# Optimization experiments

Hardware: AMD Instinct MI355X
Metric: run time of the kernel (lower is better)

Reference implementation:

```python
import jax, jax.numpy as jnp
import numpy as np

B, TS, TW = 32, 16, 16
SENT_H, WORD_H, CDIM, WDIM = 256, 512, 32, 300
VOCAB, ABJAD = 50000, 48
DIN = 2 * SENT_H   # sentence-encoder output dim
DQ = 2 * WORD_H    # word(char)-encoder output dim
DEC_H = 2 * WORD_H
DEC_IN = DIN + DQ + 8


def _lstm_dir(x, Wx, Wh, b, reverse=False):
    # x: [N, T, Din]; Wx: [4H, Din]; Wh: [4H, H]; gates ordered i,f,g,o
    pre = jnp.einsum('btd,gd->btg', x, Wx) + b
    N, H = x.shape[0], Wh.shape[1]
    h0 = jnp.zeros((N, H), x.dtype)
    def step(carry, g_in):
        h, c = carry
        g = g_in + h @ Wh.T
        i, f, gg, o = jnp.split(g, 4, axis=-1)
        c = jax.nn.sigmoid(f) * c + jax.nn.sigmoid(i) * jnp.tanh(gg)
        h = jax.nn.sigmoid(o) * jnp.tanh(c)
        return (h, c), h
    _, hs = jax.lax.scan(step, (h0, h0), jnp.swapaxes(pre, 0, 1), reverse=reverse)
    return jnp.swapaxes(hs, 0, 1)


def _bidir(x, Wx, Wh, b):
    return jnp.concatenate([_lstm_dir(x, Wx[0], Wh[0], b[0], False),
                            _lstm_dir(x, Wx[1], Wh[1], b[1], True)], axis=-1)


def setup_inputs():
    key = jax.random.key(0)
    ks = iter(jax.random.split(key, 40))
    def w(shape):
        return jax.random.normal(next(ks), shape, jnp.float32) * 0.02
    inp = {}
    inp['sents'] = jax.random.randint(next(ks), (B, TS), 0, VOCAB)
    inp['words'] = jax.random.randint(next(ks), (B, TS, TW), 0, ABJAD)
    inp['labels'] = jax.random.randint(next(ks), (B, TS, TW, 8), 0, 2)
    inp['word_embs'] = w((VOCAB, WDIM))
    inp['char_table'] = w((ABJAD, CDIM)).at[0].set(0.0)  # padding_idx=0
    inp['sent_Wx0'] = w((2, 4 * SENT_H, WDIM))
    inp['sent_Wh0'] = w((2, 4 * SENT_H, SENT_H))
    inp['sent_b0'] = jnp.zeros((2, 4 * SENT_H), jnp.float32)
    inp['sent_Wx1'] = w((2, 4 * SENT_H, 2 * SENT_H))
    inp['sent_Wh1'] = w((2, 4 * SENT_H, SENT_H))
    inp['sent_b1'] = jnp.zeros((2, 4 * SENT_H), jnp.float32)
    inp['word_Wx0'] = w((2, 4 * WORD_H, CDIM + DIN))
    inp['word_Wh0'] = w((2, 4 * WORD_H, WORD_H))
    inp['word_b0'] = jnp.zeros((2, 4 * WORD_H), jnp.float32)
    inp['word_Wx1'] = w((2, 4 * WORD_H, 2 * WORD_H))
    inp['word_Wh1'] = w((2, 4 * WORD_H, WORD_H))
    inp['word_b1'] = jnp.zeros((2, 4 * WORD_H), jnp.float32)
    inp['attn_Wq'] = w((DQ, DIN))
    inp['dec_Wx'] = w((4 * DEC_H, DEC_IN))
    inp['dec_Wh'] = w((4 * DEC_H, DEC_H))
    inp['dec_b'] = jnp.zeros((4 * DEC_H,), jnp.float32)
    inp['cls_W'] = w((DEC_H, 15))
    inp['cls_b'] = jnp.zeros((15,), jnp.float32)
    return inp


def reference(sents, words, labels, word_embs, char_table, sent_Wx0, sent_Wh0, sent_b0, sent_Wx1, sent_Wh1, sent_b1, word_Wx0, word_Wh0, word_b0, word_Wx1, word_Wh1, word_b1, attn_Wq, dec_Wx, dec_Wh, dec_b, cls_W, cls_b):
    Bb = sents.shape[0]
    word_mask = (words != 0).astype(jnp.float32)               # [B, TS, TW]
    wembs = word_embs[sents]                                   # [B, TS, 300]
    h = _bidir(wembs, sent_Wx0, sent_Wh0, sent_b0)
    sent_enc = _bidir(h, sent_Wx1, sent_Wh1, sent_b1)          # [B, TS, DIN]
    sentword = sent_enc[:, :, None, :] * word_mask[..., None]  # [B, TS, TW, DIN]
    cembs = char_table[words]                                  # [B, TS, TW, CDIM]
    char_in = jnp.concatenate([cembs, sentword], axis=-1).reshape(Bb * TS, TW, CDIM + DIN)
    h = _bidir(char_in, word_Wx0, word_Wh0, word_b0)
    char_enc = _bidir(h, word_Wx1, word_Wh1, word_b1)          # [B*TS, TW, DQ]
    char_enc_r = char_enc.reshape(Bb, TS, TW, DQ)
    # dot attention: char queries projected into sentence-encoding space, keys = sent_enc
    q = jnp.einsum('bicq,qd->bicd', char_enc_r, attn_Wq)
    scores = jnp.einsum('bicd,bjd->bicj', q, sent_enc)         # [B, TS, TW, TS]
    key_valid = (words != 0).any(-1)                           # [B, TS]
    omit_self = ~jnp.eye(TS, dtype=bool)                       # prejudice mask
    valid = key_valid[:, None, None, :] & omit_self[None, :, None, :]
    attn_map = jax.nn.softmax(jnp.where(valid, scores, -1e9), axis=-1)
    attn_enc = jnp.einsum('bicj,bjd->bicd', attn_map, sent_enc)  # [B, TS, TW, DIN]
    final = jnp.concatenate([attn_enc, char_enc_r, labels.astype(jnp.float32)], axis=-1)
    final = final.reshape(Bb, TS * TW, DEC_IN)
    dec_out = _lstm_dir(final, dec_Wx, dec_Wh, dec_b)          # [B, TS*TW, DEC_H]
    diac = dec_out @ cls_W + cls_b
    return diac.reshape(Bb, TS, TW, 15), attn_map
```

## Files before the change

kernel.cpp:

```cpp
#include <hip/hip_runtime.h>
#include <math.h>


typedef __attribute__((ext_vector_type(8))) __bf16 bf16x8;
typedef __attribute__((ext_vector_type(4))) float f32x4;
typedef __attribute__((ext_vector_type(4))) unsigned u32x4;

__device__ __forceinline__ float sigf(float x) { return 1.0f / (1.0f + expf(-x)); }

__device__ __forceinline__ unsigned short bf16rn(float x) {
  unsigned u = __float_as_uint(x);
  return (unsigned short)((u + 0x7fffu + ((u >> 16) & 1u)) >> 16);
}
__device__ __forceinline__ void splitf(float x, unsigned short& h, unsigned short& l) {
  h = bf16rn(x);
  float fh = __uint_as_float((unsigned)h << 16);
  l = bf16rn(x - fh);
}

__device__ __forceinline__ void ldg16_cc(u32x4& d, const void* p) {
  asm volatile("global_load_dwordx4 %0, %1, off sc0 sc1" : "=v"(d) : "v"(p));
}

#define FMA16(a, b, acc)                                                           \
  acc[0][0] += a.x * b.x; acc[0][1] += a.x * b.y; acc[0][2] += a.x * b.z; acc[0][3] += a.x * b.w; \
  acc[1][0] += a.y * b.x; acc[1][1] += a.y * b.y; acc[1][2] += a.y * b.z; acc[1][3] += a.y * b.w; \
  acc[2][0] += a.z * b.x; acc[2][1] += a.z * b.y; acc[2][2] += a.z * b.z; acc[2][3] += a.z * b.w; \
  acc[3][0] += a.w * b.x; acc[3][1] += a.w * b.y; acc[3][2] += a.w * b.z; acc[3][3] += a.w * b.w;

__global__ __launch_bounds__(256) void transpose_k(const float* __restrict__ in,
                                                   float* __restrict__ out,
                                                   int R, int C, int H) {
  __shared__ float tile[32][33];
  int r0 = blockIdx.x * 32, c0 = blockIdx.y * 32;
  int tx = threadIdx.x & 31, ty = threadIdx.x >> 5;
  for (int yy = ty; yy < 32; yy += 8) {
    int r = r0 + yy, c = c0 + tx;
    float v = 0.f;
    if (r < R && c < C) {
      int gs = H ? ((r & 3) * H + (r >> 2)) : r;
      v = in[(long)gs * C + c];
    }
    tile[yy][tx] = v;
  }
  __syncthreads();
  for (int yy = ty; yy < 32; yy += 8) {
    int c = c0 + yy, r = r0 + tx;
    if (r < R && c < C) out[(long)c * R + r] = tile[tx][yy];
  }
}

__global__ void embed_k(const int* __restrict__ sents, const float* __restrict__ word_embs,
                        float* __restrict__ wembs) {
  int idx = blockIdx.x * 256 + threadIdx.x;
  if (idx >= 512 * 300) return;
  int r = idx / 300, k = idx - r * 300;
  wembs[idx] = word_embs[(long)sents[r] * 300 + k];
}

__global__ void charin_k(const int* __restrict__ words, const float* __restrict__ char_table,
                         const float* __restrict__ sent_enc,
                         unsigned short* __restrict__ ciH, unsigned short* __restrict__ ciL) {
  int idx = blockIdx.x * 256 + threadIdx.x;
  if (idx >= 512 * 16 * 544) return;
  int k = idx % 544;
  int rc = idx / 544;
  int c = rc & 15, n = rc >> 4;
  int w = words[n * 16 + c];
  float v;
  if (k < 32) v = char_table[w * 32 + k];
  else v = (w != 0) ? sent_enc[n * 512 + (k - 32)] : 0.f;
  unsigned short h, l;
  splitf(v, h, l);
  ciH[idx] = h; ciL[idx] = l;
}

__global__ void labels_k(const int* __restrict__ labels,
                         unsigned short* __restrict__ fH, unsigned short* __restrict__ fL) {
  int idx = blockIdx.x * 256 + threadIdx.x;
  if (idx >= 8192 * 8) return;
  int r = idx >> 3, l = idx & 7;
  long o = (long)r * 1544 + 1536 + l;
  fH[o] = bf16rn((float)labels[idx]);
  fL[o] = 0;
}

__global__ void decwh_prep_k(const float* __restrict__ dec_Wh,
                             unsigned short* __restrict__ WhFH,
                             unsigned short* __restrict__ WhFL) {
  long o = (long)blockIdx.x * 256 + threadIdx.x;
  if (o >= 4194304) return;
  int j = (int)(o & 7);
  int lane = (int)((o >> 3) & 63);
  int kt = (int)((o >> 9) & 31);
  int nt = (int)(o >> 14);
  int col = nt * 16 + (lane & 15);
  int gsrc = (col & 3) * 1024 + (col >> 2);
  int k = kt * 32 + ((lane >> 4) & 3) * 8 + j;
  float v = dec_Wh[(long)gsrc * 1024 + k];
  unsigned short h, l;
  splitf(v, h, l);
  WhFH[o] = h; WhFL[o] = l;
}

template <int HASBIAS>
__global__ __launch_bounds__(256) void gemm_k(const float* __restrict__ A, int lda,
                                              const float* __restrict__ Bw,
                                              const float* __restrict__ bias,
                                              float* __restrict__ C, int ldc,
                                              int M, int N, int K) {
  __shared__ float As[32][64];
  __shared__ float Bs[32][64];
  int tid = threadIdx.x;
  int m0 = blockIdx.x * 64, n0 = blockIdx.y * 64;
  int tn = tid & 15, tm = tid >> 4;
  int lrow = tid >> 2, lk = (tid & 3) * 8;
  float acc[4][4] = {};
  int am = m0 + lrow;
  const float* aptr = A + (long)am * lda;
  bool mok = am < M;
  int bn = n0 + lrow;
  const float* bptr = Bw + (long)bn * K;
  bool nok = bn < N;

  for (int k0 = 0; k0 < K; k0 += 32) {
    int kb = k0 + lk;
    if (kb + 8 <= K) {
      if (mok) {
        float4 v0 = *(const float4*)(aptr + kb);
        float4 v1 = *(const float4*)(aptr + kb + 4);
        As[lk + 0][lrow] = v0.x; As[lk + 1][lrow] = v0.y; As[lk + 2][lrow] = v0.z; As[lk + 3][lrow] = v0.w;
        As[lk + 4][lrow] = v1.x; As[lk + 5][lrow] = v1.y; As[lk + 6][lrow] = v1.z; As[lk + 7][lrow] = v1.w;
      } else {
#pragma unroll
        for (int i = 0; i < 8; i++) As[lk + i][lrow] = 0.f;
      }
      if (nok) {
        float4 v0 = *(const float4*)(bptr + kb);
        float4 v1 = *(const float4*)(bptr + kb + 4);
        Bs[lk + 0][lrow] = v0.x; Bs[lk + 1][lrow] = v0.y; Bs[lk + 2][lrow] = v0.z; Bs[lk + 3][lrow] = v0.w;
        Bs[lk + 4][lrow] = v1.x; Bs[lk + 5][lrow] = v1.y; Bs[lk + 6][lrow] = v1.z; Bs[lk + 7][lrow] = v1.w;
      } else {
#pragma unroll
        for (int i = 0; i < 8; i++) Bs[lk + i][lrow] = 0.f;
      }
    } else {
#pragma unroll
      for (int i = 0; i < 8; i++) {
        int k = kb + i;
        As[lk + i][lrow] = (mok && k < K) ? aptr[k] : 0.f;
        Bs[lk + i][lrow] = (nok && k < K) ? bptr[k] : 0.f;
      }
    }
    __syncthreads();
#pragma unroll
    for (int kk = 0; kk < 32; kk++) {
      float4 a = *(const float4*)&As[kk][tm * 4];
      float4 b = *(const float4*)&Bs[kk][tn * 4];
      FMA16(a, b, acc)
    }
    __syncthreads();
  }
#pragma unroll
  for (int i = 0; i < 4; i++) {
    int m = m0 + tm * 4 + i;
    if (m >= M) continue;
#pragma unroll
    for (int j = 0; j < 4; j++) {
      int n = n0 + tn * 4 + j;
      if (n >= N) continue;
      float v = acc[i][j];
      if (HASBIAS) v += bias[n];
      C[(long)m * ldc + n] = v;
    }
  }
}

template <int AMODE, int BH, int HASBIAS>
__global__ __launch_bounds__(256) void mgemm_k(const unsigned short* __restrict__ AH,
                                               const unsigned short* __restrict__ AL,
                                               int lda, int at0,
                                               const float* __restrict__ B,
                                               const float* __restrict__ bias,
                                               float* __restrict__ C, int ldc, int K) {
  __shared__ __align__(16) unsigned short Ah[64 * 40], Al[64 * 40], Bh[64 * 40], Bl[64 * 40];
  int tid = threadIdx.x;
  int m0 = blockIdx.x * 64, n0 = blockIdx.y * 64;
  int srow = tid >> 2, skoff = (tid & 3) * 8;
  int am = m0 + srow;
  long arow = (AMODE == 1) ? ((long)(am & 31) * 256 + at0 + (am >> 5)) : (long)am;
  const unsigned short* aptrH = AH + arow * (long)lda;
  const unsigned short* aptrL = AL + arow * (long)lda;
  int bn = n0 + srow;
  long gsrc;
  if (BH > 0) gsrc = (long)(bn & 3) * BH + (bn >> 2);
  else gsrc = bn;
  const float* bptr = B + gsrc * (long)K;

  int lane = tid & 63, wv = tid >> 6;
  int wm = (wv >> 1) * 32, wn = (wv & 1) * 32;
  int fr = lane & 15, fk = (lane >> 4) * 8;
  int rbase = (lane >> 4) * 4;

  f32x4 acc[2][2] = {};
  for (int k0 = 0; k0 < K; k0 += 32) {
    int kb = k0 + skoff;
    uint4 vh, vl;
    unsigned short hb[8] __attribute__((aligned(16))), lb[8] __attribute__((aligned(16)));
    if (kb + 8 <= K) {
      vh = *(const uint4*)(aptrH + kb);
      vl = *(const uint4*)(aptrL + kb);
      float4 b0 = *(const float4*)(bptr + kb);
      float4 b1 = *(const float4*)(bptr + kb + 4);
      float bv[8] = {b0.x, b0.y, b0.z, b0.w, b1.x, b1.y, b1.z, b1.w};
#pragma unroll
      for (int e = 0; e < 8; e++) splitf(bv[e], hb[e], lb[e]);
    } else {
      unsigned short ea[8] __attribute__((aligned(16))), el[8] __attribute__((aligned(16)));
#pragma unroll
      for (int e = 0; e < 8; e++) {
        int k = kb + e;
        ea[e] = (k < K) ? aptrH[k] : 0;
        el[e] = (k < K) ? aptrL[k] : 0;
        float bvv = (k < K) ? bptr[k] : 0.f;
        splitf(bvv, hb[e], lb[e]);
      }
      vh = *(const uint4*)ea;
      vl = *(const uint4*)el;
    }
    __syncthreads();
    *(uint4*)&Ah[srow * 40 + skoff] = vh;
    *(uint4*)&Al[srow * 40 + skoff] = vl;
    *(uint4*)&Bh[srow * 40 + skoff] = *(const uint4*)hb;
    *(uint4*)&Bl[srow * 40 + skoff] = *(const uint4*)lb;
    __syncthreads();
    bf16x8 fah[2], fal[2], fbh[2], fbl[2];
#pragma unroll
    for (int i = 0; i < 2; i++) {
      fah[i] = *(const bf16x8*)&Ah[(wm + i * 16 + fr) * 40 + fk];
      fal[i] = *(const bf16x8*)&Al[(wm + i * 16 + fr) * 40 + fk];
      fbh[i] = *(const bf16x8*)&Bh[(wn + i * 16 + fr) * 40 + fk];
      fbl[i] = *(const bf16x8*)&Bl[(wn + i * 16 + fr) * 40 + fk];
    }
#pragma unroll
    for (int i = 0; i < 2; i++)
#pragma unroll
      for (int j = 0; j < 2; j++) {
        acc[i][j] = __builtin_amdgcn_mfma_f32_16x16x32_bf16(fah[i], fbh[j], acc[i][j], 0, 0, 0);
        acc[i][j] = __builtin_amdgcn_mfma_f32_16x16x32_bf16(fah[i], fbl[j], acc[i][j], 0, 0, 0);
        acc[i][j] = __builtin_amdgcn_mfma_f32_16x16x32_bf16(fal[i], fbh[j], acc[i][j], 0, 0, 0);
      }
  }
#pragma unroll
  for (int i = 0; i < 2; i++)
#pragma unroll
    for (int j = 0; j < 2; j++)
#pragma unroll
      for (int r = 0; r < 4; r++) {
        int m = m0 + wm + i * 16 + rbase + r;
        int n = n0 + wn + j * 16 + fr;
        float v = acc[i][j][r];
        if (HASBIAS) {
          long gs = (BH > 0) ? ((long)(n & 3) * BH + (n >> 2)) : (long)n;
          v += bias[gs];
        }
        C[(long)m * ldc + n] = v;
      }
}

template <int K1>
__global__ __launch_bounds__(256) void mstep_k(
    const unsigned short* __restrict__ xFH, const unsigned short* __restrict__ xFL,
    const unsigned short* __restrict__ xBH, const unsigned short* __restrict__ xBL,
    int xstride,
    const float* __restrict__ Wx, const float* __restrict__ Wh,
    const float* __restrict__ bias,
    const unsigned short* __restrict__ hInH, const unsigned short* __restrict__ hInL,
    unsigned short* __restrict__ hOutH, unsigned short* __restrict__ hOutL,
    float* __restrict__ c_st,
    unsigned short* __restrict__ outH, unsigned short* __restrict__ outL,
    int out_stride, int tF, int tB) {
  __shared__ __align__(16) char smem[20480];
  unsigned short* Ah = (unsigned short*)smem;
  unsigned short* Al = Ah + 2560;
  unsigned short* Bh = Ah + 5120;
  unsigned short* Bl = Ah + 7680;
  float* gbuf = (float*)smem;

  int tid = threadIdx.x;
  int m0 = blockIdx.x * 64, n0 = blockIdx.y * 64;
  int dir = n0 >> 11;
  int nn0 = n0 & 2047;
  int srow = tid >> 2, skoff = (tid & 3) * 8;

  int am = m0 + srow;
  const unsigned short* axH = dir ? xBH : xFH;
  const unsigned short* axL = dir ? xBL : xFL;
  const unsigned short* arow_xH = axH + (long)am * xstride;
  const unsigned short* arow_xL = axL + (long)am * xstride;
  const unsigned short* arow_hH = hInH + (long)dir * 262144 + (long)am * 512;
  const unsigned short* arow_hL = hInL + (long)dir * 262144 + (long)am * 512;

  int bn = nn0 + srow;
  long gsrc = (long)dir * 2048 + (bn & 3) * 512 + (bn >> 2);
  const float* brow_x = Wx + gsrc * (long)K1;
  const float* brow_h = Wh + gsrc * 512L;

  int lane = tid & 63, wv = tid >> 6;
  int wm = (wv >> 1) * 32, wn = (wv & 1) * 32;
  int fr = lane & 15, fk = (lane >> 4) * 8;
  int rbase = (lane >> 4) * 4;

  f32x4 acc[2][2] = {};
  const int K = K1 + 512;
  for (int k0 = 0; k0 < K; k0 += 32) {
    int kb = k0 + skoff;
    uint4 vh, vl;
    const float* bp;
    if (kb < K1) {
      vh = *(const uint4*)(arow_xH + kb);
      vl = *(const uint4*)(arow_xL + kb);
      bp = brow_x + kb;
    } else {
      vh = *(const uint4*)(arow_hH + (kb - K1));
      vl = *(const uint4*)(arow_hL + (kb - K1));
      bp = brow_h + (kb - K1);
    }
    float4 b0 = *(const float4*)bp;
    float4 b1 = *(const float4*)(bp + 4);
    float bv[8] = {b0.x, b0.y, b0.z, b0.w, b1.x, b1.y, b1.z, b1.w};
    unsigned short hb[8] __attribute__((aligned(16))), lb[8] __attribute__((aligned(16)));
#pragma unroll
    for (int e = 0; e < 8; e++) splitf(bv[e], hb[e], lb[e]);
    __syncthreads();
    *(uint4*)&Ah[srow * 40 + skoff] = vh;
    *(uint4*)&Al[srow * 40 + skoff] = vl;
    *(uint4*)&Bh[srow * 40 + skoff] = *(const uint4*)hb;
    *(uint4*)&Bl[srow * 40 + skoff] = *(const uint4*)lb;
    __syncthreads();
    bf16x8 fah[2], fal[2], fbh[2], fbl[2];
#pragma unroll
    for (int i = 0; i < 2; i++) {
      fah[i] = *(const bf16x8*)&Ah[(wm + i * 16 + fr) * 40 + fk];
      fal[i] = *(const bf16x8*)&Al[(wm + i * 16 + fr) * 40 + fk];
      fbh[i] = *(const bf16x8*)&Bh[(wn + i * 16 + fr) * 40 + fk];
      fbl[i] = *(const bf16x8*)&Bl[(wn + i * 16 + fr) * 40 + fk];
    }
#pragma unroll
    for (int i = 0; i < 2; i++)
#pragma unroll
      for (int j = 0; j < 2; j++) {
        acc[i][j] = __builtin_amdgcn_mfma_f32_16x16x32_bf16(fah[i], fbh[j], acc[i][j], 0, 0, 0);
        acc[i][j] = __builtin_amdgcn_mfma_f32_16x16x32_bf16(fah[i], fbl[j], acc[i][j], 0, 0, 0);
        acc[i][j] = __builtin_amdgcn_mfma_f32_16x16x32_bf16(fal[i], fbh[j], acc[i][j], 0, 0, 0);
      }
  }
  __syncthreads();
#pragma unroll
  for (int i = 0; i < 2; i++)
#pragma unroll
    for (int j = 0; j < 2; j++)
#pragma unroll
      for (int r = 0; r < 4; r++)
        gbuf[(wm + i * 16 + rbase + r) * 68 + (wn + j * 16 + fr)] = acc[i][j][r];
  __syncthreads();

  int ug0 = nn0 >> 2;
  int t = dir ? tB : tF;
  for (int it = tid; it < 1024; it += 256) {
    int r = it >> 4, ul = it & 15;
    int seq = m0 + r, ug = ug0 + ul;
    float gi = gbuf[r * 68 + ul * 4 + 0] + bias[dir * 2048 + ug];
    float gf = gbuf[r * 68 + ul * 4 + 1] + bias[dir * 2048 + 512 + ug];
    float gg = gbuf[r * 68 + ul * 4 + 2] + bias[dir * 2048 + 1024 + ug];
    float go = gbuf[r * 68 + ul * 4 + 3] + bias[dir * 2048 + 1536 + ug];
    long ci = (long)dir * 262144 + (long)seq * 512 + ug;
    float c = sigf(gf) * c_st[ci] + sigf(gi) * tanhf(gg);
    float h = sigf(go) * tanhf(c);
    c_st[ci] = c;
    unsigned short hh, hl;
    splitf(h, hh, hl);
    hOutH[ci] = hh;
    hOutL[ci] = hl;
    long oo = ((long)seq * 16 + t) * out_stride + dir * 512 + ug;
    outH[oo] = hh;
    outL[oo] = hl;
  }
}

__global__ __launch_bounds__(256) void sent_rec_k(const float* __restrict__ pre,
                                                  const float* __restrict__ WhT,
                                                  float* __restrict__ out) {
  int blk = blockIdx.x;
  int n = blk & 31, dir = blk >> 5;
  int tid = threadIdx.x;
  __shared__ float hls[256];
  __shared__ float gls[1024];
  float c = 0.f;
  hls[tid] = 0.f;
  __syncthreads();
  const float* whbase = WhT + (long)dir * 256 * 1024;
  int g4 = tid * 4;
  for (int s = 0; s < 16; s++) {
    int t = dir ? (15 - s) : s;
    const float* prow = pre + (long)(n * 16 + t) * 2048 + dir * 1024;
    float ax = 0.f, ay = 0.f, az = 0.f, aw = 0.f;
#pragma unroll 4
    for (int k = 0; k < 256; k++) {
      float hk = hls[k];
      float4 w = *(const float4*)(whbase + (long)k * 1024 + g4);
      ax += hk * w.x; ay += hk * w.y; az += hk * w.z; aw += hk * w.w;
    }
    float4 p = *(const float4*)(prow + g4);
    gls[g4 + 0] = ax + p.x; gls[g4 + 1] = ay + p.y;
    gls[g4 + 2] = az + p.z; gls[g4 + 3] = aw + p.w;
    __syncthreads();
    float gi = gls[tid], gf = gls[256 + tid], gg = gls[512 + tid], go = gls[768 + tid];
    c = sigf(gf) * c + sigf(gi) * tanhf(gg);
    float h = sigf(go) * tanhf(c);
    __syncthreads();
    hls[tid] = h;
    out[(long)n * 8192 + (long)t * 512 + dir * 256 + tid] = h;
    __syncthreads();
  }
}

__global__ __launch_bounds__(256, 1) void dec_persist_k(
    const unsigned short* __restrict__ WhFH, const unsigned short* __restrict__ WhFL,
    const float* __restrict__ pre,
    unsigned short* __restrict__ hH, unsigned short* __restrict__ hL,
    float* __restrict__ c_st, float* __restrict__ dec_out,
    int* __restrict__ cnt, int tbase) {
  extern __shared__ char smem[];
  unsigned short* wHs = (unsigned short*)smem;
  unsigned short* wLs = (unsigned short*)(smem + 65536);
  float* gbuf = (float*)(smem + 131072);

  int tid = threadIdx.x, bid = blockIdx.x;
  int lane = tid & 63, kh = tid >> 6;
  int fr = lane & 15, fq = (lane >> 4) & 3;
  int grp = bid >> 3;

  {
    const unsigned short* gH = WhFH + (long)bid * 32768;
    const unsigned short* gL = WhFL + (long)bid * 32768;
    for (int o = tid * 8; o < 32768; o += 2048) {
      *(uint4*)&wHs[o] = *(const uint4*)&gH[o];
      *(uint4*)&wLs[o] = *(const uint4*)&gL[o];
    }
  }

  int bb = tid >> 2, up = tid & 3;
  int u0 = bid * 8 + up * 2;
  long co = (long)bb * 1024 + u0;
  float c0 = 0.f, c1 = 0.f;
  if (tid < 128) {
    float2 cc = *(const float2*)&c_st[co];
    c0 = cc.x;
    c1 = cc.y;
  }
  __syncthreads();

  for (int tl = 0; tl < 32; tl++) {
    int t = tbase + tl;
    const unsigned short* hInH = hH + (long)(t & 1) * 32768;
    const unsigned short* hInL = hL + (long)(t & 1) * 32768;
    unsigned short* hOutH = hH + (long)((t + 1) & 1) * 32768;
    unsigned short* hOutL = hL + (long)((t + 1) & 1) * 32768;

    float4 p0 = {0.f, 0.f, 0.f, 0.f}, p1 = {0.f, 0.f, 0.f, 0.f};
    if (tid < 128) {
      const float* pr = pre + ((long)tl * 32 + bb) * 4096 + bid * 32 + up * 8;
      p0 = *(const float4*)pr;
      p1 = *(const float4*)(pr + 4);
    }

    u32x4 hHr[2][8], hLr[2][8];
#pragma unroll
    for (int bh = 0; bh < 2; bh++)
#pragma unroll
      for (int i = 0; i < 8; i++) {
        long a = (long)(bh * 16 + fr) * 1024 + (kh * 8 + i) * 32 + fq * 8;
        ldg16_cc(hHr[bh][i], hInH + a);
        ldg16_cc(hLr[bh][i], hInL + a);
      }
    asm volatile("s_waitcnt vmcnt(0)");
    __builtin_amdgcn_sched_barrier(0);

    f32x4 acc[2][2] = {};
#pragma unroll
    for (int i = 0; i < 8; i++) {
      int kt = kh * 8 + i;
#pragma unroll
      for (int ct = 0; ct < 2; ct++) {
        bf16x8 wh = *(const bf16x8*)&wHs[(ct * 32 + kt) * 512 + lane * 8];
        bf16x8 wl = *(const bf16x8*)&wLs[(ct * 32 + kt) * 512 + lane * 8];
#pragma unroll
        for (int bh = 0; bh < 2; bh++) {
          bf16x8 ah = __builtin_bit_cast(bf16x8, hHr[bh][i]);
          bf16x8 al = __builtin_bit_cast(bf16x8, hLr[bh][i]);
          acc[ct][bh] = __builtin_amdgcn_mfma_f32_16x16x32_bf16(ah, wh, acc[ct][bh], 0, 0, 0);
          acc[ct][bh] = __builtin_amdgcn_mfma_f32_16x16x32_bf16(ah, wl, acc[ct][bh], 0, 0, 0);
          acc[ct][bh] = __builtin_amdgcn_mfma_f32_16x16x32_bf16(al, wh, acc[ct][bh], 0, 0, 0);
        }
      }
    }
#pragma unroll
    for (int ct = 0; ct < 2; ct++)
#pragma unroll
      for (int bh = 0; bh < 2; bh++)
#pragma unroll
        for (int r = 0; r < 4; r++)
          gbuf[(kh * 32 + bh * 16 + fq * 4 + r) * 33 + ct * 16 + fr] = acc[ct][bh][r];
    __syncthreads();

    if (tid < 128) {
      float g[8];
#pragma unroll
      for (int e = 0; e < 8; e++) {
        float s = gbuf[bb * 33 + up * 8 + e];
#pragma unroll
        for (int q = 1; q < 4; q++) s += gbuf[(q * 32 + bb) * 33 + up * 8 + e];
        g[e] = s;
      }
      c0 = sigf(g[1] + p0.y) * c0 + sigf(g[0] + p0.x) * tanhf(g[2] + p0.z);
      float h0 = sigf(g[3] + p0.w) * tanhf(c0);
      c1 = sigf(g[5] + p1.y) * c1 + sigf(g[4] + p1.x) * tanhf(g[6] + p1.z);
      float h1 = sigf(g[7] + p1.w) * tanhf(c1);
      unsigned short h0h, h0l, h1h, h1l;
      splitf(h0, h0h, h0l);
      splitf(h1, h1h, h1l);
      unsigned ph = (unsigned)h0h | ((unsigned)h1h << 16);
      unsigned pl = (unsigned)h0l | ((unsigned)h1l << 16);
      __hip_atomic_store((unsigned*)(hOutH + co), ph, __ATOMIC_RELAXED,
                         __HIP_MEMORY_SCOPE_AGENT);
      __hip_atomic_store((unsigned*)(hOutL + co), pl, __ATOMIC_RELAXED,
                         __HIP_MEMORY_SCOPE_AGENT);
      float2 hv;
      hv.x = h0;
      hv.y = h1;
      *(float2*)&dec_out[((long)bb * 256 + t) * 1024 + u0] = hv;
    }
    __syncthreads();

    if (tl < 31) {
      if (tid == 0) {
        int old = __hip_atomic_fetch_add(&cnt[grp * 32], 1, __ATOMIC_RELAXED,
                                         __HIP_MEMORY_SCOPE_AGENT);
        if (old == 8 * tl + 7)
          __hip_atomic_fetch_add(&cnt[512], 1, __ATOMIC_RELAXED,
                                 __HIP_MEMORY_SCOPE_AGENT);
        while (__hip_atomic_load(&cnt[512], __ATOMIC_RELAXED,
                                 __HIP_MEMORY_SCOPE_AGENT) < 16 * (tl + 1))
          __builtin_amdgcn_s_sleep(1);
      }
      __syncthreads();
    }
  }
  if (tid < 128) {
    float2 cv;
    cv.x = c0;
    cv.y = c1;
    *(float2*)&c_st[co] = cv;
  }
}

__global__ __launch_bounds__(256) void attn_k(const float* __restrict__ sent_enc,
                                              const float* __restrict__ qbuf,
                                              const int* __restrict__ words,
                                              float* __restrict__ attn_out,
                                              unsigned short* __restrict__ fH,
                                              unsigned short* __restrict__ fL) {
  int b = blockIdx.x >> 4;
  int i = blockIdx.x & 15;
  int tid = threadIdx.x;
  __shared__ float se[16][512];
  __shared__ float qq[16][512];
  __shared__ float sc[16][16];
  __shared__ int kv[16];
  if (tid < 16) kv[tid] = 0;
  __syncthreads();
  {
    int j = tid >> 4, c = tid & 15;
    if (words[(b * 16 + j) * 16 + c] != 0) atomicOr(&kv[j], 1);
  }
  for (int idx = tid; idx < 16 * 128; idx += 256) {
    int j = idx >> 7, d4 = idx & 127;
    *(float4*)&se[j][d4 * 4] = *(const float4*)(sent_enc + (long)(b * 16 + j) * 512 + d4 * 4);
  }
  for (int idx = tid; idx < 16 * 128; idx += 256) {
    int c = idx >> 7, d4 = idx & 127;
    *(float4*)&qq[c][d4 * 4] = *(const float4*)(qbuf + (long)(b * 256 + i * 16 + c) * 512 + d4 * 4);
  }
  __syncthreads();
  int c = tid >> 4, j = tid & 15;
  {
    float s = 0.f;
#pragma unroll 4
    for (int k = 0; k < 512; k++) s += qq[c][k] * se[j][k];
    bool valid = (kv[j] != 0) && (j != i);
    sc[c][j] = valid ? s : -1e9f;
  }
  __syncthreads();
  float m = -INFINITY;
#pragma unroll
  for (int t = 0; t < 16; t++) m = fmaxf(m, sc[c][t]);
  float den = 0.f;
#pragma unroll
  for (int t = 0; t < 16; t++) den += expf(sc[c][t] - m);
  float a = expf(sc[c][j] - m) / den;
  __syncthreads();
  sc[c][j] = a;
  attn_out[((long)((b * 16 + i) * 16 + c)) * 16 + j] = a;
  __syncthreads();
  {
    int part = tid & 15;
    int cc = tid >> 4;
    for (int d = part * 32; d < part * 32 + 32; d++) {
      float v = 0.f;
#pragma unroll
      for (int jj = 0; jj < 16; jj++) v += sc[cc][jj] * se[jj][d];
      long o = (long)(b * 256 + i * 16 + cc) * 1544 + d;
      unsigned short hh, hl;
      splitf(v, hh, hl);
      fH[o] = hh;
      fL[o] = hl;
    }
  }
}

extern "C" void kernel_launch(void* const* d_in, const int* in_sizes, int n_in,
                              void* d_out, int out_size, void* d_ws, size_t ws_size,
                              hipStream_t stream) {
  const int* sents = (const int*)d_in[0];
  const int* words = (const int*)d_in[1];
  const int* labels = (const int*)d_in[2];
  const float* word_embs = (const float*)d_in[3];
  const float* char_table = (const float*)d_in[4];
  const float* sent_Wx0 = (const float*)d_in[5];
  const float* sent_Wh0 = (const float*)d_in[6];
  const float* sent_b0 = (const float*)d_in[7];
  const float* sent_Wx1 = (const float*)d_in[8];
  const float* sent_Wh1 = (const float*)d_in[9];
  const float* sent_b1 = (const float*)d_in[10];
  const float* word_Wx0 = (const float*)d_in[11];
  const float* word_Wh0 = (const float*)d_in[12];
  const float* word_b0 = (const float*)d_in[13];
  const float* word_Wx1 = (const float*)d_in[14];
  const float* word_Wh1 = (const float*)d_in[15];
  const float* word_b1 = (const float*)d_in[16];
  const float* attn_Wq = (const float*)d_in[17];
  const float* dec_Wx = (const float*)d_in[18];
  const float* dec_Wh = (const float*)d_in[19];
  const float* dec_b = (const float*)d_in[20];
  const float* cls_W = (const float*)d_in[21];
  const float* cls_b = (const float*)d_in[22];

  char* base = (char*)d_ws;
  float* wembs   = (float*)(base + 0);
  float* preS    = (float*)(base + 614400);
  float* hs0     = (float*)(base + 4808704);
  float* WhT0    = (float*)(base + 5857280);
  float* WhT1    = (float*)(base + 7954432);
  float* sentenc = (float*)(base + 10051584);
  unsigned short* hcharH = (unsigned short*)(base + 11100160);
  unsigned short* hcharL = (unsigned short*)(base + 13197312);
  float* cchar   = (float*)(base + 15294464);
  unsigned short* WhFH = (unsigned short*)(base + 0);
  unsigned short* WhFL = (unsigned short*)(base + 8388608);
  unsigned short* finalbH = (unsigned short*)(base + 17391616);
  unsigned short* finalbL = (unsigned short*)(base + 42688512);
  float* qbuf = (float*)(base + 67985408);
  float* pre  = qbuf;
  float* WqT = (float*)(base + 84762624);
  unsigned short* charinH = (unsigned short*)(base + 86859776);
  unsigned short* charinL = (unsigned short*)(base + 95772672);
  unsigned short* hc0H = (unsigned short*)(base + 104685568);
  unsigned short* hc0L = (unsigned short*)(base + 121462784);
  float* dec_out = (float*)(base + 86859776);
  unsigned short* hdecH = (unsigned short*)(base + 120414208);
  unsigned short* hdecL = (unsigned short*)(base + 120545280);
  float* c_dec = (float*)(base + 120676352);
  float* clsWT = (float*)(base + 120807424);
  int* cnt = (int*)(base + 120868864);

  float* dout = (float*)d_out;
  float* diac = dout;
  float* attnmap = dout + 122880;

  static bool s_dec_attr = false;
  if (!s_dec_attr) {
    hipFuncSetAttribute(reinterpret_cast<const void*>(dec_persist_k),
                        hipFuncAttributeMaxDynamicSharedMemorySize, 147968);
    s_dec_attr = true;
  }

  transpose_k<<<dim3(32, 8), 256, 0, stream>>>(sent_Wh0, WhT0, 1024, 256, 0);
  transpose_k<<<dim3(32, 8), 256, 0, stream>>>(sent_Wh0 + 262144, WhT0 + 262144, 1024, 256, 0);
  transpose_k<<<dim3(32, 8), 256, 0, stream>>>(sent_Wh1, WhT1, 1024, 256, 0);
  transpose_k<<<dim3(32, 8), 256, 0, stream>>>(sent_Wh1 + 262144, WhT1 + 262144, 1024, 256, 0);
  transpose_k<<<dim3(32, 16), 256, 0, stream>>>(attn_Wq, WqT, 1024, 512, 0);

  embed_k<<<600, 256, 0, stream>>>(sents, word_embs, wembs);
  gemm_k<1><<<dim3(8, 32), 256, 0, stream>>>(wembs, 300, sent_Wx0, sent_b0,
                                             preS, 2048, 512, 2048, 300);
  sent_rec_k<<<64, 256, 0, stream>>>(preS, WhT0, hs0);
  gemm_k<1><<<dim3(8, 32), 256, 0, stream>>>(hs0, 512, sent_Wx1, sent_b1,
                                             preS, 2048, 512, 2048, 512);
  sent_rec_k<<<64, 256, 0, stream>>>(preS, WhT1, sentenc);

  charin_k<<<17408, 256, 0, stream>>>(words, char_table, sentenc, charinH, charinL);

  hipMemsetAsync(base + 11100160, 0, 6291456, stream);
  for (int s = 0; s < 16; s++) {
    int p = s & 1;
    mstep_k<544><<<dim3(8, 64), 256, 0, stream>>>(
        charinH + s * 544, charinL + s * 544,
        charinH + (15 - s) * 544, charinL + (15 - s) * 544, 16 * 544,
        word_Wx0, word_Wh0, word_b0,
        hcharH + p * 524288, hcharL + p * 524288,
        hcharH + (p ^ 1) * 524288, hcharL + (p ^ 1) * 524288, cchar,
        hc0H, hc0L, 1024, s, 15 - s);
  }
  hipMemsetAsync(base + 11100160, 0, 6291456, stream);
  for (int s = 0; s < 16; s++) {
    int p = s & 1;
    mstep_k<1024><<<dim3(8, 64), 256, 0, stream>>>(
        hc0H + s * 1024, hc0L + s * 1024,
        hc0H + (15 - s) * 1024, hc0L + (15 - s) * 1024, 16 * 1024,
        word_Wx1, word_Wh1, word_b1,
        hcharH + p * 524288, hcharL + p * 524288,
        hcharH + (p ^ 1) * 524288, hcharL + (p ^ 1) * 524288, cchar,
        finalbH + 512, finalbL + 512, 1544, s, 15 - s);
  }

  mgemm_k<0, 0, 0><<<dim3(128, 8), 256, 0, stream>>>(finalbH + 512, finalbL + 512, 1544, 0,
                                                     WqT, nullptr, qbuf, 512, 1024);
  attn_k<<<512, 256, 0, stream>>>(sentenc, qbuf, words, attnmap, finalbH, finalbL);
  labels_k<<<256, 256, 0, stream>>>(labels, finalbH, finalbL);

  decwh_prep_k<<<16384, 256, 0, stream>>>(dec_Wh, WhFH, WhFL);
  hipMemsetAsync(base + 120414208, 0, 393216, stream);
  for (int ch = 0; ch < 8; ch++) {
    mgemm_k<1, 1024, 1><<<dim3(16, 64), 256, 0, stream>>>(finalbH, finalbL, 1544, ch * 32,
                                                          dec_Wx, dec_b, pre, 4096, 1544);
    hipMemsetAsync(cnt, 0, 4096, stream);
    dec_persist_k<<<128, 256, 147968, stream>>>(WhFH, WhFL, pre, hdecH, hdecL,
                                                c_dec, dec_out, cnt, ch * 32);
  }

  transpose_k<<<dim3(32, 1), 256, 0, stream>>>(cls_W, clsWT, 1024, 15, 0);
  gemm_k<1><<<dim3(128, 1), 256, 0, stream>>>(dec_out, 1024, clsWT, cls_b,
                                              diac, 15, 8192, 15, 1024);
}
```

Before: 4.701 ms.

## Shrink decoder persistent grid to 32 larger blocks reading Wh from global

The decoder recurrence kernel moves from 128 blocks of 256 threads, each holding its Wh slice in LDS, to 32 blocks of 512 threads that each handle four times as many hidden units. Weights are now read from global memory (L2) every timestep instead of being staged in LDS. The grid barrier drops from a two-level counter to a single counter over 32 blocks. The aim is cheaper cross-block synchronisation per step, at the cost of re-reading the full Wh from cache every step and running on fewer CUs.

Result: slower. 7.208 ms (+53.3%).

```diff
diff --git a/kernel.cpp b/kernel.cpp
--- a/kernel.cpp
+++ b/kernel.cpp
@@ -425,41 +425,26 @@
   }
 }
 
-__global__ __launch_bounds__(256, 1) void dec_persist_k(
+__global__ __launch_bounds__(512, 2) void dec_persist_k(
     const unsigned short* __restrict__ WhFH, const unsigned short* __restrict__ WhFL,
     const float* __restrict__ pre,
     unsigned short* __restrict__ hH, unsigned short* __restrict__ hL,
     float* __restrict__ c_st, float* __restrict__ dec_out,
     int* __restrict__ cnt, int tbase) {
   extern __shared__ char smem[];
-  unsigned short* wHs = (unsigned short*)smem;
-  unsigned short* wLs = (unsigned short*)(smem + 65536);
-  float* gbuf = (float*)(smem + 131072);
+  float* gbuf = (float*)smem;
 
   int tid = threadIdx.x, bid = blockIdx.x;
   int lane = tid & 63, kh = tid >> 6;
   int fr = lane & 15, fq = (lane >> 4) & 3;
-  int grp = bid >> 3;
-
-  {
-    const unsigned short* gH = WhFH + (long)bid * 32768;
-    const unsigned short* gL = WhFL + (long)bid * 32768;
-    for (int o = tid * 8; o < 32768; o += 2048) {
-      *(uint4*)&wHs[o] = *(const uint4*)&gH[o];
-      *(uint4*)&wLs[o] = *(const uint4*)&gL[o];
-    }
-  }
-
-  int bb = tid >> 2, up = tid & 3;
-  int u0 = bid * 8 + up * 2;
+
+  int bb = tid >> 4, up = tid & 15;
+  int u0 = bid * 32 + up * 2;
   long co = (long)bb * 1024 + u0;
-  float c0 = 0.f, c1 = 0.f;
-  if (tid < 128) {
-    float2 cc = *(const float2*)&c_st[co];
-    c0 = cc.x;
-    c1 = cc.y;
-  }
-  __syncthreads();
+  float2 cc = *(const float2*)&c_st[co];
+  float c0 = cc.x, c1 = cc.y;
+
+  const long wfb = ((long)(bid * 8) * 32 + kh * 4) * 512 + lane * 8;
 
   for (int tl = 0; tl < 32; tl++) {
     int t = tbase + tl;
@@ -468,33 +453,32 @@
     unsigned short* hOutH = hH + (long)((t + 1) & 1) * 32768;
     unsigned short* hOutL = hL + (long)((t + 1) & 1) * 32768;
 
-    float4 p0 = {0.f, 0.f, 0.f, 0.f}, p1 = {0.f, 0.f, 0.f, 0.f};
-    if (tid < 128) {
-      const float* pr = pre + ((long)tl * 32 + bb) * 4096 + bid * 32 + up * 8;
-      p0 = *(const float4*)pr;
-      p1 = *(const float4*)(pr + 4);
-    }
-
-    u32x4 hHr[2][8], hLr[2][8];
+    const float* pr = pre + ((long)tl * 32 + bb) * 4096 + bid * 128 + up * 8;
+    float4 p0 = *(const float4*)pr;
+    float4 p1 = *(const float4*)(pr + 4);
+
+    u32x4 hHr[2][4], hLr[2][4];
 #pragma unroll
     for (int bh = 0; bh < 2; bh++)
 #pragma unroll
-      for (int i = 0; i < 8; i++) {
-        long a = (long)(bh * 16 + fr) * 1024 + (kh * 8 + i) * 32 + fq * 8;
+      for (int i = 0; i < 4; i++) {
+        long a = (long)(bh * 16 + fr) * 1024 + (kh * 4 + i) * 32 + fq * 8;
         ldg16_cc(hHr[bh][i], hInH + a);
         ldg16_cc(hLr[bh][i], hInL + a);
       }
     asm volatile("s_waitcnt vmcnt(0)");
     __builtin_amdgcn_sched_barrier(0);
 
-    f32x4 acc[2][2] = {};
-#pragma unroll
-    for (int i = 0; i < 8; i++) {
-      int kt = kh * 8 + i;
-#pragma unroll
-      for (int ct = 0; ct < 2; ct++) {
-        bf16x8 wh = *(const bf16x8*)&wHs[(ct * 32 + kt) * 512 + lane * 8];
-        bf16x8 wl = *(const bf16x8*)&wLs[(ct * 32 + kt) * 512 + lane * 8];
+    f32x4 acc[8][2] = {};
+#pragma unroll
+    for (int i = 0; i < 4; i++) {
+      long wk = wfb + (long)i * 512;
+#pragma unroll
+      for (int ct = 0; ct < 8; ct++) {
+        u32x4 whv = *(const u32x4*)&WhFH[wk + (long)ct * 16384];
+        u32x4 wlv = *(const u32x4*)&WhFL[wk + (long)ct * 16384];
+        bf16x8 wh = __builtin_bit_cast(bf16x8, whv);
+        bf16x8 wl = __builtin_bit_cast(bf16x8, wlv);
 #pragma unroll
         for (int bh = 0; bh < 2; bh++) {
           bf16x8 ah = __builtin_bit_cast(bf16x8, hHr[bh][i]);
@@ -506,21 +490,21 @@
       }
     }
 #pragma unroll
-    for (int ct = 0; ct < 2; ct++)
+    for (int ct = 0; ct < 8; ct++)
 #pragma unroll
       for (int bh = 0; bh < 2; bh++)
 #pragma unroll
         for (int r = 0; r < 4; r++)
-          gbuf[(kh * 32 + bh * 16 + fq * 4 + r) * 33 + ct * 16 + fr] = acc[ct][bh][r];
-    __syncthreads();
-
-    if (tid < 128) {
+          gbuf[(kh * 32 + bh * 16 + fq * 4 + r) * 132 + ct * 16 + fr] = acc[ct][bh][r];
+    __syncthreads();
+
+    {
       float g[8];
 #pragma unroll
       for (int e = 0; e < 8; e++) {
-        float s = gbuf[bb * 33 + up * 8 + e];
-#pragma unroll
-        for (int q = 1; q < 4; q++) s += gbuf[(q * 32 + bb) * 33 + up * 8 + e];
+        float s = 0.f;
+#pragma unroll
+        for (int q = 0; q < 8; q++) s += gbuf[(q * 32 + bb) * 132 + up * 8 + e];
         g[e] = s;
       }
       c0 = sigf(g[1] + p0.y) * c0 + sigf(g[0] + p0.x) * tanhf(g[2] + p0.z);
@@ -545,19 +529,16 @@
 
     if (tl < 31) {
       if (tid == 0) {
-        int old = __hip_atomic_fetch_add(&cnt[grp * 32], 1, __ATOMIC_RELAXED,
-                                         __HIP_MEMORY_SCOPE_AGENT);
-        if (old == 8 * tl + 7)
-          __hip_atomic_fetch_add(&cnt[512], 1, __ATOMIC_RELAXED,
-                                 __HIP_MEMORY_SCOPE_AGENT);
-        while (__hip_atomic_load(&cnt[512], __ATOMIC_RELAXED,
-                                 __HIP_MEMORY_SCOPE_AGENT) < 16 * (tl + 1))
+        __hip_atomic_fetch_add(&cnt[0], 1, __ATOMIC_RELAXED,
+                               __HIP_MEMORY_SCOPE_AGENT);
+        while (__hip_atomic_load(&cnt[0], __ATOMIC_RELAXED,
+                                 __HIP_MEMORY_SCOPE_AGENT) < 32 * (tl + 1))
           __builtin_amdgcn_s_sleep(1);
       }
       __syncthreads();
     }
   }
-  if (tid < 128) {
+  {
     float2 cv;
     cv.x = c0;
     cv.y = c1;
@@ -691,7 +672,7 @@
   static bool s_dec_attr = false;
   if (!s_dec_attr) {
     hipFuncSetAttribute(reinterpret_cast<const void*>(dec_persist_k),
-                        hipFuncAttributeMaxDynamicSharedMemorySize, 147968);
+                        hipFuncAttributeMaxDynamicSharedMemorySize, 135168);
     s_dec_attr = true;
   }
 
@@ -745,8 +726,8 @@
     mgemm_k<1, 1024, 1><<<dim3(16, 64), 256, 0, stream>>>(finalbH, finalbL, 1544, ch * 32,
                                                           dec_Wx, dec_b, pre, 4096, 1544);
     hipMemsetAsync(cnt, 0, 4096, stream);
-    dec_persist_k<<<128, 256, 147968, stream>>>(WhFH, WhFL, pre, hdecH, hdecL,
-                                                c_dec, dec_out, cnt, ch * 32);
+    dec_persist_k<<<32, 512, 135168, stream>>>(WhFH, WhFL, pre, hdecH, hdecL,
+                                               c_dec, dec_out, cnt, ch * 32);
   }
 
   transpose_k<<<dim3(32, 1), 256, 0, stream>>>(cls_W, clsWT, 1024, 15, 0);
```

## Overlap next-chunk decoder input GEMM with recurrent decoder via extra blocks

Applied to the files above, without the earlier changes.

The persistent decoder kernel gains 128 extra blocks. While the first 128 blocks run the recurrence for the current 32-step chunk, the extra blocks compute the next chunk's input-projection GEMM into a second, double-buffered pre-activation buffer. This takes the separate per-chunk GEMM launch off the serial path, and the sync counter now runs continuously across chunks, so only one memset is needed. The cost is that the GEMM blocks compete for memory bandwidth with the latency-bound recurrence. It also relies on all 256 blocks being co-resident and on the new pre1 buffer not overlapping live data.

Result: no change. 4.752 ms (+1.1%).

```diff
diff --git a/kernel.cpp b/kernel.cpp
--- a/kernel.cpp
+++ b/kernel.cpp
@@ -425,143 +425,233 @@
   }
 }
 
-__global__ __launch_bounds__(256, 1) void dec_persist_k(
+__global__ __launch_bounds__(256, 1) void dec_fused_k(
     const unsigned short* __restrict__ WhFH, const unsigned short* __restrict__ WhFL,
     const float* __restrict__ pre,
     unsigned short* __restrict__ hH, unsigned short* __restrict__ hL,
     float* __restrict__ c_st, float* __restrict__ dec_out,
-    int* __restrict__ cnt, int tbase) {
+    int* __restrict__ cnt, int tbase,
+    const unsigned short* __restrict__ AH, const unsigned short* __restrict__ AL,
+    const float* __restrict__ Bw, const float* __restrict__ bias,
+    float* __restrict__ pre_nxt, int at0, int do_gemm) {
   extern __shared__ char smem[];
-  unsigned short* wHs = (unsigned short*)smem;
-  unsigned short* wLs = (unsigned short*)(smem + 65536);
-  float* gbuf = (float*)(smem + 131072);
-
   int tid = threadIdx.x, bid = blockIdx.x;
-  int lane = tid & 63, kh = tid >> 6;
-  int fr = lane & 15, fq = (lane >> 4) & 3;
-  int grp = bid >> 3;
-
-  {
-    const unsigned short* gH = WhFH + (long)bid * 32768;
-    const unsigned short* gL = WhFL + (long)bid * 32768;
-    for (int o = tid * 8; o < 32768; o += 2048) {
-      *(uint4*)&wHs[o] = *(const uint4*)&gH[o];
-      *(uint4*)&wLs[o] = *(const uint4*)&gL[o];
-    }
-  }
-
-  int bb = tid >> 2, up = tid & 3;
-  int u0 = bid * 8 + up * 2;
-  long co = (long)bb * 1024 + u0;
-  float c0 = 0.f, c1 = 0.f;
-  if (tid < 128) {
-    float2 cc = *(const float2*)&c_st[co];
-    c0 = cc.x;
-    c1 = cc.y;
-  }
-  __syncthreads();
-
-  for (int tl = 0; tl < 32; tl++) {
-    int t = tbase + tl;
-    const unsigned short* hInH = hH + (long)(t & 1) * 32768;
-    const unsigned short* hInL = hL + (long)(t & 1) * 32768;
-    unsigned short* hOutH = hH + (long)((t + 1) & 1) * 32768;
-    unsigned short* hOutL = hL + (long)((t + 1) & 1) * 32768;
-
-    float4 p0 = {0.f, 0.f, 0.f, 0.f}, p1 = {0.f, 0.f, 0.f, 0.f};
+
+  if (bid < 128) {
+    unsigned short* wHs = (unsigned short*)smem;
+    unsigned short* wLs = (unsigned short*)(smem + 65536);
+    float* gbuf = (float*)(smem + 131072);
+
+    int lane = tid & 63, kh = tid >> 6;
+    int fr = lane & 15, fq = (lane >> 4) & 3;
+    int grp = bid >> 3;
+
+    {
+      const unsigned short* gH = WhFH + (long)bid * 32768;
+      const unsigned short* gL = WhFL + (long)bid * 32768;
+      for (int o = tid * 8; o < 32768; o += 2048) {
+        *(uint4*)&wHs[o] = *(const uint4*)&gH[o];
+        *(uint4*)&wLs[o] = *(const uint4*)&gL[o];
+      }
+    }
+
+    int bb = tid >> 2, up = tid & 3;
+    int u0 = bid * 8 + up * 2;
+    long co = (long)bb * 1024 + u0;
+    float c0 = 0.f, c1 = 0.f;
     if (tid < 128) {
-      const float* pr = pre + ((long)tl * 32 + bb) * 4096 + bid * 32 + up * 8;
-      p0 = *(const float4*)pr;
-      p1 = *(const float4*)(pr + 4);
-    }
-
-    u32x4 hHr[2][8], hLr[2][8];
-#pragma unroll
-    for (int bh = 0; bh < 2; bh++)
+      float2 cc = *(const float2*)&c_st[co];
+      c0 = cc.x;
+      c1 = cc.y;
+    }
+    __syncthreads();
+
+    for (int tl = 0; tl < 32; tl++) {
+      int t = tbase + tl;
+      const unsigned short* hInH = hH + (long)(t & 1) * 32768;
+      const unsigned short* hInL = hL + (long)(t & 1) * 32768;
+      unsigned short* hOutH = hH + (long)((t + 1) & 1) * 32768;
+      unsigned short* hOutL = hL + (long)((t + 1) & 1) * 32768;
+
+      float4 p0 = {0.f, 0.f, 0.f, 0.f}, p1 = {0.f, 0.f, 0.f, 0.f};
+      if (tid < 128) {
+        const float* pr = pre + ((long)tl * 32 + bb) * 4096 + bid * 32 + up * 8;
+        p0 = *(const float4*)pr;
+        p1 = *(const float4*)(pr + 4);
+      }
+
+      u32x4 hHr[2][8], hLr[2][8];
+#pragma unroll
+      for (int bh = 0; bh < 2; bh++)
+#pragma unroll
+        for (int i = 0; i < 8; i++) {
+          long a = (long)(bh * 16 + fr) * 1024 + (kh * 8 + i) * 32 + fq * 8;
+          ldg16_cc(hHr[bh][i], hInH + a);
+          ldg16_cc(hLr[bh][i], hInL + a);
+        }
+      asm volatile("s_waitcnt vmcnt(0)");
+      __builtin_amdgcn_sched_barrier(0);
+
+      f32x4 acc[2][2] = {};
 #pragma unroll
       for (int i = 0; i < 8; i++) {
-        long a = (long)(bh * 16 + fr) * 1024 + (kh * 8 + i) * 32 + fq * 8;
-        ldg16_cc(hHr[bh][i], hInH + a);
-        ldg16_cc(hLr[bh][i], hInL + a);
-      }
-    asm volatile("s_waitcnt vmcnt(0)");
-    __builtin_amdgcn_sched_barrier(0);
-
-    f32x4 acc[2][2] = {};
-#pragma unroll
-    for (int i = 0; i < 8; i++) {
-      int kt = kh * 8 + i;
-#pragma unroll
-      for (int ct = 0; ct < 2; ct++) {
-        bf16x8 wh = *(const bf16x8*)&wHs[(ct * 32 + kt) * 512 + lane * 8];
-        bf16x8 wl = *(const bf16x8*)&wLs[(ct * 32 + kt) * 512 + lane * 8];
-#pragma unroll
-        for (int bh = 0; bh < 2; bh++) {
-          bf16x8 ah = __builtin_bit_cast(bf16x8, hHr[bh][i]);
-          bf16x8 al = __builtin_bit_cast(bf16x8, hLr[bh][i]);
-          acc[ct][bh] = __builtin_amdgcn_mfma_f32_16x16x32_bf16(ah, wh, acc[ct][bh], 0, 0, 0);
-          acc[ct][bh] = __builtin_amdgcn_mfma_f32_16x16x32_bf16(ah, wl, acc[ct][bh], 0, 0, 0);
-          acc[ct][bh] = __builtin_amdgcn_mfma_f32_16x16x32_bf16(al, wh, acc[ct][bh], 0, 0, 0);
+        int kt = kh * 8 + i;
+#pragma unroll
+        for (int ct = 0; ct < 2; ct++) {
+          bf16x8 wh = *(const bf16x8*)&wHs[(ct * 32 + kt) * 512 + lane * 8];
+          bf16x8 wl = *(const bf16x8*)&wLs[(ct * 32 + kt) * 512 + lane * 8];
+#pragma unroll
+          for (int bh = 0; bh < 2; bh++) {
+            bf16x8 ah = __builtin_bit_cast(bf16x8, hHr[bh][i]);
+            bf16x8 al = __builtin_bit_cast(bf16x8, hLr[bh][i]);
+            acc[ct][bh] = __builtin_amdgcn_mfma_f32_16x16x32_bf16(ah, wh, acc[ct][bh], 0, 0, 0);
+            acc[ct][bh] = __builtin_amdgcn_mfma_f32_16x16x32_bf16(ah, wl, acc[ct][bh], 0, 0, 0);
+            acc[ct][bh] = __builtin_amdgcn_mfma_f32_16x16x32_bf16(al, wh, acc[ct][bh], 0, 0, 0);
+          }
         }
       }
-    }
-#pragma unroll
-    for (int ct = 0; ct < 2; ct++)
-#pragma unroll
-      for (int bh = 0; bh < 2; bh++)
-#pragma unroll
-        for (int r = 0; r < 4; r++)
-          gbuf[(kh * 32 + bh * 16 + fq * 4 + r) * 33 + ct * 16 + fr] = acc[ct][bh][r];
-    __syncthreads();
-
-    if (tid < 128) {
-      float g[8];
-#pragma unroll
-      for (int e = 0; e < 8; e++) {
-        float s = gbuf[bb * 33 + up * 8 + e];
-#pragma unroll
-        for (int q = 1; q < 4; q++) s += gbuf[(q * 32 + bb) * 33 + up * 8 + e];
-        g[e] = s;
-      }
-      c0 = sigf(g[1] + p0.y) * c0 + sigf(g[0] + p0.x) * tanhf(g[2] + p0.z);
-      float h0 = sigf(g[3] + p0.w) * tanhf(c0);
-      c1 = sigf(g[5] + p1.y) * c1 + sigf(g[4] + p1.x) * tanhf(g[6] + p1.z);
-      float h1 = sigf(g[7] + p1.w) * tanhf(c1);
-      unsigned short h0h, h0l, h1h, h1l;
-      splitf(h0, h0h, h0l);
-      splitf(h1, h1h, h1l);
-      unsigned ph = (unsigned)h0h | ((unsigned)h1h << 16);
-      unsigned pl = (unsigned)h0l | ((unsigned)h1l << 16);
-      __hip_atomic_store((unsigned*)(hOutH + co), ph, __ATOMIC_RELAXED,
-                         __HIP_MEMORY_SCOPE_AGENT);
-      __hip_atomic_store((unsigned*)(hOutL + co), pl, __ATOMIC_RELAXED,
-                         __HIP_MEMORY_SCOPE_AGENT);
-      float2 hv;
-      hv.x = h0;
-      hv.y = h1;
-      *(float2*)&dec_out[((long)bb * 256 + t) * 1024 + u0] = hv;
-    }
-    __syncthreads();
-
-    if (tl < 31) {
+#pragma unroll
+      for (int ct = 0; ct < 2; ct++)
+#pragma unroll
+        for (int bh = 0; bh < 2; bh++)
+#pragma unroll
+          for (int r = 0; r < 4; r++)
+            gbuf[(kh * 32 + bh * 16 + fq * 4 + r) * 33 + ct * 16 + fr] = acc[ct][bh][r];
+      __syncthreads();
+
+      if (tid < 128) {
+        float g[8];
+#pragma unroll
+        for (int e = 0; e < 8; e++) {
+          float s = gbuf[bb * 33 + up * 8 + e];
+#pragma unroll
+          for (int q = 1; q < 4; q++) s += gbuf[(q * 32 + bb) * 33 + up * 8 + e];
+          g[e] = s;
+        }
+        c0 = sigf(g[1] + p0.y) * c0 + sigf(g[0] + p0.x) * tanhf(g[2] + p0.z);
+        float h0 = sigf(g[3] + p0.w) * tanhf(c0);
+        c1 = sigf(g[5] + p1.y) * c1 + sigf(g[4] + p1.x) * tanhf(g[6] + p1.z);
+        float h1 = sigf(g[7] + p1.w) * tanhf(c1);
+        unsigned short h0h, h0l, h1h, h1l;
+        splitf(h0, h0h, h0l);
+        splitf(h1, h1h, h1l);
+        unsigned ph = (unsigned)h0h | ((unsigned)h1h << 16);
+        unsigned pl = (unsigned)h0l | ((unsigned)h1l << 16);
+        __hip_atomic_store((unsigned*)(hOutH + co), ph, __ATOMIC_RELAXED,
+                           __HIP_MEMORY_SCOPE_AGENT);
+        __hip_atomic_store((unsigned*)(hOutL + co), pl, __ATOMIC_RELAXED,
+                           __HIP_MEMORY_SCOPE_AGENT);
+        float2 hv;
+        hv.x = h0;
+        hv.y = h1;
+        *(float2*)&dec_out[((long)bb * 256 + t) * 1024 + u0] = hv;
+      }
+      __syncthreads();
+
       if (tid == 0) {
         int old = __hip_atomic_fetch_add(&cnt[grp * 32], 1, __ATOMIC_RELAXED,
                                          __HIP_MEMORY_SCOPE_AGENT);
-        if (old == 8 * tl + 7)
+        if (old == 8 * t + 7)
           __hip_atomic_fetch_add(&cnt[512], 1, __ATOMIC_RELAXED,
                                  __HIP_MEMORY_SCOPE_AGENT);
         while (__hip_atomic_load(&cnt[512], __ATOMIC_RELAXED,
-                                 __HIP_MEMORY_SCOPE_AGENT) < 16 * (tl + 1))
+                                 __HIP_MEMORY_SCOPE_AGENT) < 16 * (t + 1))
           __builtin_amdgcn_s_sleep(1);
       }
       __syncthreads();
     }
-  }
-  if (tid < 128) {
-    float2 cv;
-    cv.x = c0;
-    cv.y = c1;
-    *(float2*)&c_st[co] = cv;
+    if (tid < 128) {
+      float2 cv;
+      cv.x = c0;
+      cv.y = c1;
+      *(float2*)&c_st[co] = cv;
+    }
+  } else if (do_gemm) {
+    unsigned short* Ah = (unsigned short*)smem;
+    unsigned short* Al = Ah + 2560;
+    unsigned short* Bh = Ah + 5120;
+    unsigned short* Bl = Ah + 7680;
+    const int K = 1544;
+    int srow = tid >> 2, skoff = (tid & 3) * 8;
+    int lane = tid & 63, wv = tid >> 6;
+    int wm = (wv >> 1) * 32, wn = (wv & 1) * 32;
+    int fr = lane & 15, fk = (lane >> 4) * 8;
+    int rbase = (lane >> 4) * 4;
+    int gid = bid - 128;
+
+    for (int t8 = 0; t8 < 8; t8++) {
+      int tile = gid + 128 * t8;
+      int m0 = (tile & 15) * 64, n0 = (tile >> 4) * 64;
+      int am = m0 + srow;
+      long arow = (long)(am & 31) * 256 + at0 + (am >> 5);
+      const unsigned short* aptrH = AH + arow * 1544L;
+      const unsigned short* aptrL = AL + arow * 1544L;
+      int bn = n0 + srow;
+      long gsrc = (long)(bn & 3) * 1024 + (bn >> 2);
+      const float* bptr = Bw + gsrc * 1544L;
+
+      f32x4 acc[2][2] = {};
+      for (int k0 = 0; k0 < K; k0 += 32) {
+        int kb = k0 + skoff;
+        uint4 vh, vl;
+        unsigned short hb[8] __attribute__((aligned(16))), lb[8] __attribute__((aligned(16)));
+        if (kb + 8 <= K) {
+          vh = *(const uint4*)(aptrH + kb);
+          vl = *(const uint4*)(aptrL + kb);
+          float4 b0 = *(const float4*)(bptr + kb);
+          float4 b1 = *(const float4*)(bptr + kb + 4);
+          float bv[8] = {b0.x, b0.y, b0.z, b0.w, b1.x, b1.y, b1.z, b1.w};
+#pragma unroll
+          for (int e = 0; e < 8; e++) splitf(bv[e], hb[e], lb[e]);
+        } else {
+          unsigned short ea[8] __attribute__((aligned(16))), el[8] __attribute__((aligned(16)));
+#pragma unroll
+          for (int e = 0; e < 8; e++) {
+            int k = kb + e;
+            ea[e] = (k < K) ? aptrH[k] : 0;
+            el[e] = (k < K) ? aptrL[k] : 0;
+            float bvv = (k < K) ? bptr[k] : 0.f;
+            splitf(bvv, hb[e], lb[e]);
+          }
+          vh = *(const uint4*)ea;
+          vl = *(const uint4*)el;
+        }
+        __syncthreads();
+        *(uint4*)&Ah[srow * 40 + skoff] = vh;
+        *(uint4*)&Al[srow * 40 + skoff] = vl;
+        *(uint4*)&Bh[srow * 40 + skoff] = *(const uint4*)hb;
+        *(uint4*)&Bl[srow * 40 + skoff] = *(const uint4*)lb;
+        __syncthreads();
+        bf16x8 fah[2], fal[2], fbh[2], fbl[2];
+#pragma unroll
+        for (int i = 0; i < 2; i++) {
+          fah[i] = *(const bf16x8*)&Ah[(wm + i * 16 + fr) * 40 + fk];
+          fal[i] = *(const bf16x8*)&Al[(wm + i * 16 + fr) * 40 + fk];
+          fbh[i] = *(const bf16x8*)&Bh[(wn + i * 16 + fr) * 40 + fk];
+          fbl[i] = *(const bf16x8*)&Bl[(wn + i * 16 + fr) * 40 + fk];
+        }
+#pragma unroll
+        for (int i = 0; i < 2; i++)
+#pragma unroll
+          for (int j = 0; j < 2; j++) {
+            acc[i][j] = __builtin_amdgcn_mfma_f32_16x16x32_bf16(fah[i], fbh[j], acc[i][j], 0, 0, 0);
+            acc[i][j] = __builtin_amdgcn_mfma_f32_16x16x32_bf16(fah[i], fbl[j], acc[i][j], 0, 0, 0);
+            acc[i][j] = __builtin_amdgcn_mfma_f32_16x16x32_bf16(fal[i], fbh[j], acc[i][j], 0, 0, 0);
+          }
+      }
+#pragma unroll
+      for (int i = 0; i < 2; i++)
+#pragma unroll
+        for (int j = 0; j < 2; j++)
+#pragma unroll
+          for (int r = 0; r < 4; r++) {
+            int m = m0 + wm + i * 16 + rbase + r;
+            int n = n0 + wn + j * 16 + fr;
+            long gs = (long)(n & 3) * 1024 + (n >> 2);
+            pre_nxt[(long)m * 4096 + n] = acc[i][j][r] + bias[gs];
+          }
+      __syncthreads();
+    }
   }
 }
 
@@ -671,7 +761,7 @@
   unsigned short* finalbH = (unsigned short*)(base + 17391616);
   unsigned short* finalbL = (unsigned short*)(base + 42688512);
   float* qbuf = (float*)(base + 67985408);
-  float* pre  = qbuf;
+  float* pre0 = qbuf;
   float* WqT = (float*)(base + 84762624);
   unsigned short* charinH = (unsigned short*)(base + 86859776);
   unsigned short* charinL = (unsigned short*)(base + 95772672);
@@ -683,6 +773,7 @@
   float* c_dec = (float*)(base + 120676352);
   float* clsWT = (float*)(base + 120807424);
   int* cnt = (int*)(base + 120868864);
+  float* pre1 = (float*)(base + 121462784);
 
   float* dout = (float*)d_out;
   float* diac = dout;
@@ -690,7 +781,7 @@
 
   static bool s_dec_attr = false;
   if (!s_dec_attr) {
-    hipFuncSetAttribute(reinterpret_cast<const void*>(dec_persist_k),
+    hipFuncSetAttribute(reinterpret_cast<const void*>(dec_fused_k),
                         hipFuncAttributeMaxDynamicSharedMemorySize, 147968);
     s_dec_attr = true;
   }
@@ -741,12 +832,15 @@
 
   decwh_prep_k<<<16384, 256, 0, stream>>>(dec_Wh, WhFH, WhFL);
   hipMemsetAsync(base + 120414208, 0, 393216, stream);
+  hipMemsetAsync(cnt, 0, 4096, stream);
+  mgemm_k<1, 1024, 1><<<dim3(16, 64), 256, 0, stream>>>(finalbH, finalbL, 1544, 0,
+                                                        dec_Wx, dec_b, pre0, 4096, 1544);
+  float* preBuf[2] = {pre0, pre1};
   for (int ch = 0; ch < 8; ch++) {
-    mgemm_k<1, 1024, 1><<<dim3(16, 64), 256, 0, stream>>>(finalbH, finalbL, 1544, ch * 32,
-                                                          dec_Wx, dec_b, pre, 4096, 1544);
-    hipMemsetAsync(cnt, 0, 4096, stream);
-    dec_persist_k<<<128, 256, 147968, stream>>>(WhFH, WhFL, pre, hdecH, hdecL,
-                                                c_dec, dec_out, cnt, ch * 32);
+    dec_fused_k<<<256, 256, 147968, stream>>>(
+        WhFH, WhFL, preBuf[ch & 1], hdecH, hdecL, c_dec, dec_out, cnt, ch * 32,
+        finalbH, finalbL, dec_Wx, dec_b, preBuf[(ch + 1) & 1], (ch + 1) * 32,
+        (ch < 7) ? 1 : 0);
   }
 
   transpose_k<<<dim3(32, 1), 256, 0, stream>>>(cls_W, clsWT, 1024, 15, 0);
```
